# Kernel optimization log

Measured on AMD Instinct MI355X. Metric: run time of the kernel, lower is better.

The kernel has to match this reference:

```python
import jax, jax.numpy as jnp
import numpy as np

NEG_INF = -1e9

def _build_tables():
    # LC0-style 73-plane encoding per from-square: planes 0..55 queen moves
    # (8 directions x 7 distances), 56..63 knight moves. to_sq[from, plane]
    # is the to-square index; valid marks on-board targets.
    to_sq = np.zeros((64, 64), np.int32)
    valid = np.zeros((64, 64), bool)
    dirs = [(1, 0), (1, 1), (0, 1), (-1, 1), (-1, 0), (-1, -1), (0, -1), (1, -1)]
    knights = [(2, 1), (1, 2), (-1, 2), (-2, 1), (-2, -1), (-1, -2), (1, -2), (2, -1)]
    for sq in range(64):
        r, c = divmod(sq, 8)
        for d, (dr, dc) in enumerate(dirs):
            for dist in range(1, 8):
                p = d * 7 + (dist - 1)
                nr, nc = r + dr * dist, c + dc * dist
                if 0 <= nr < 8 and 0 <= nc < 8:
                    to_sq[sq, p] = nr * 8 + nc
                    valid[sq, p] = True
        for i, (dr, dc) in enumerate(knights):
            nr, nc = r + dr, c + dc
            if 0 <= nr < 8 and 0 <= nc < 8:
                to_sq[sq, 56 + i] = nr * 8 + nc
                valid[sq, 56 + i] = True
    promo_from = (np.arange(64) // 8) == 6  # rank 7 pawns (0-indexed rank 6)
    return to_sq, valid, promo_from

TO_SQ_NP, VALID_NP, PROMO_FROM_NP = _build_tables()
TO_SQ = jnp.asarray(TO_SQ_NP)            # (64, 64) int32
TO_VALID = jnp.asarray(VALID_NP)         # (64, 64) bool
PROMO_FROM = jnp.asarray(PROMO_FROM_NP)  # (64,) bool

EMBED_DIM = 1024
POLICY_DIM = 128
SCALE = POLICY_DIM ** (-0.5)


def setup_inputs() -> dict:
    key = jax.random.key(0)
    ks = jax.random.split(key, 4)
    B = 1024
    std = 1.0 / np.sqrt(EMBED_DIM)
    x = jax.random.normal(ks[0], (B, 64, EMBED_DIM), dtype=jnp.float32)
    Wq = jax.random.normal(ks[1], (EMBED_DIM, POLICY_DIM), dtype=jnp.float32) * std
    Wk = jax.random.normal(ks[2], (EMBED_DIM, POLICY_DIM), dtype=jnp.float32) * std
    Wu = jax.random.normal(ks[3], (EMBED_DIM, 9), dtype=jnp.float32) * std
    bq = jnp.zeros((POLICY_DIM,), jnp.float32)
    bk = jnp.zeros((POLICY_DIM,), jnp.float32)
    bu = jnp.zeros((9,), jnp.float32)
    return {"x": x, "Wq": Wq, "bq": bq, "Wk": Wk, "bk": bk, "Wu": Wu, "bu": bu}


def reference(x, Wq, bq, Wk, bk, Wu, bu):
    b = x.shape[0]
    q = jnp.einsum('bsd,dp->bsp', x, Wq) + bq            # (B, 64, P)
    k = jnp.einsum('bsd,dp->bsp', x, Wk) + bk            # (B, 64, P)
    logits_ft = jnp.einsum('bfp,btp->bft', q, k) * SCALE  # (B, 64, 64)
    # gather to-square logits into plane order per from-square
    idx = jnp.broadcast_to(TO_SQ[None].astype(jnp.int32), (b, 64, 64))
    logits_64 = jnp.take_along_axis(logits_ft, idx, axis=-1)  # (B, 64, 64)
    logits_64 = jnp.where(TO_VALID[None], logits_64, jnp.float32(NEG_INF))
    up = jnp.einsum('bsd,dn->bsn', x, Wu) + bu            # (B, 64, 9)
    up = jnp.where(PROMO_FROM[None, :, None], up, jnp.float32(NEG_INF))
    logits = jnp.concatenate([logits_64, up], axis=-1)    # (B, 64, 73)
    return logits.reshape(b, 64 * 73)
```

## Files before the change

### kernel.cpp

```cpp
#include <hip/hip_runtime.h>

#define NEG_INF (-1e9f)
#define SCALE_F 0.08838834764831845f

typedef __attribute__((ext_vector_type(8))) short short8;
typedef __attribute__((ext_vector_type(4))) float float4v;

__device__ __constant__ int cDR[8] = {1,1,0,-1,-1,-1,0,1};
__device__ __constant__ int cDC[8] = {0,1,1,1,0,-1,-1,-1};
__device__ __constant__ int cKR[8] = {2,1,-1,-2,-2,-1,1,2};
__device__ __constant__ int cKC[8] = {1,2,2,1,-1,-2,-2,-1};

__device__ __forceinline__ ushort f2bf(float f) {
  union { float f; unsigned u; } a; a.f = f;
  unsigned u = a.u;
  return (ushort)((u + 0x7FFFu + ((u >> 16) & 1u)) >> 16);
}

__device__ __forceinline__ short8 pack8(float4 a, float4 b) {
  union { short8 v; unsigned u[4]; } o;
  unsigned a0 = __float_as_uint(a.x), a1 = __float_as_uint(a.y);
  unsigned a2 = __float_as_uint(a.z), a3 = __float_as_uint(a.w);
  unsigned b0 = __float_as_uint(b.x), b1 = __float_as_uint(b.y);
  unsigned b2 = __float_as_uint(b.z), b3 = __float_as_uint(b.w);
  o.u[0] = (a1 & 0xFFFF0000u) | (a0 >> 16);
  o.u[1] = (a3 & 0xFFFF0000u) | (a2 >> 16);
  o.u[2] = (b1 & 0xFFFF0000u) | (b0 >> 16);
  o.u[3] = (b3 & 0xFFFF0000u) | (b2 >> 16);
  return o.v;
}

__global__ void wconv_kernel(const float* __restrict__ Wq,
                             const float* __restrict__ Wk,
                             const float* __restrict__ Wu,
                             ushort* __restrict__ Wsw) {
  int row = blockIdx.x;
  for (int k = threadIdx.x; k < 1024; k += 256) {
    float v;
    if (row < 128)      v = Wq[k * 128 + row];
    else if (row < 256) v = Wk[k * 128 + (row - 128)];
    else if (row < 265) v = Wu[k * 9 + (row - 256)];
    else                v = 0.f;
    int kc = k >> 6, kin = k & 63;
    Wsw[(size_t)kc * 18432 + row * 64 + kin] = f2bf(v);
  }
}

__global__ __launch_bounds__(256, 2)
void apol_main(const float* __restrict__ x,
               const float* __restrict__ bq,
               const float* __restrict__ bk,
               const float* __restrict__ bu,
               const ushort* __restrict__ Wsw,
               float* __restrict__ out) {
  __shared__ __align__(16) char smem[65536];
  char*   xs  = smem;
  ushort* qs  = (ushort*)smem;
  ushort* ks  = (ushort*)(smem + 16896);
  float*  Sl  = (float*)smem;

  const int tid = threadIdx.x;
  const int w = tid >> 6, lane = tid & 63;
  const int l15 = lane & 15, qd = lane >> 4;
  const char* xb = (const char*)(x + (size_t)blockIdx.x * 65536);
  const char* WsB = (const char*)Wsw;

  const int arow = l15 * 1024;
  const int axor = l15 & 7;

  const int wvo = (w * 64 + l15) * 128 + qd * 16;
  const int uvo = (256 + l15) * 128 + qd * 16;

  float4v acc[4][4];
  #pragma unroll
  for (int i = 0; i < 4; ++i)
    #pragma unroll
    for (int j = 0; j < 4; ++j)
      acc[i][j] = (float4v){0.f, 0.f, 0.f, 0.f};
  float4v aup = (float4v){0.f, 0.f, 0.f, 0.f};

  for (int h = 0; h < 2; ++h) {
    if (h) __syncthreads();
    #pragma unroll 8
    for (int j = 0; j < 16; ++j) {
      int row = j * 4 + w;
      const char* s = xb + row * 4096 + h * 2048 + lane * 32;
      float4 g0 = *(const float4*)(s);
      float4 g1 = *(const float4*)(s + 16);
      *(short8*)(xs + row * 1024 + ((lane ^ (row & 7)) * 16)) = pack8(g0, g1);
    }
    __syncthreads();

    const char* wh = WsB + (size_t)h * 8 * 36864;
    #pragma unroll 2
    for (int kc8 = 0; kc8 < 8; ++kc8) {
      const char* wp = wh + kc8 * 36864;
      #pragma unroll
      for (int kk = 0; kk < 2; ++kk) {
        short8 bf[4];
        #pragma unroll
        for (int nt = 0; nt < 4; ++nt)
          bf[nt] = *(const short8*)(wp + wvo + nt * 2048 + kk * 64);
        short8 ub;
        if (w == 3) ub = *(const short8*)(wp + uvo + kk * 64);
        #pragma unroll
        for (int mt = 0; mt < 4; ++mt) {
          short8 af = *(const short8*)(
              xs + mt * 16384 + arow + (((kc8 * 8 + kk * 4 + qd) ^ axor) * 16));
          #pragma unroll
          for (int nt = 0; nt < 4; ++nt)
            acc[mt][nt] = __builtin_amdgcn_mfma_f32_16x16x32_bf16(
                af, bf[nt], acc[mt][nt], 0, 0, 0);
          if (w == 3 && mt == 3)
            aup = __builtin_amdgcn_mfma_f32_16x16x32_bf16(af, ub, aup, 0, 0, 0);
        }
      }
    }
  }
  __syncthreads();

  float* outb = out + (size_t)blockIdx.x * 4672;

  if (w == 3 && qd < 2 && l15 < 9) {
    float bias = bu[l15];
    #pragma unroll
    for (int r = 0; r < 4; ++r) {
      int f = 48 + qd * 4 + r;
      outb[f * 73 + 64 + l15] = aup[r] + bias;
    }
  }

  #pragma unroll
  for (int nt = 0; nt < 4; ++nt) {
    int C = w * 64 + nt * 16 + l15;
    bool isq = (C < 128);
    int p = isq ? C : (C - 128);
    float bias = isq ? bq[p] : bk[p];
    ushort* dstb = isq ? qs : ks;
    #pragma unroll
    for (int mt = 0; mt < 4; ++mt)
      #pragma unroll
      for (int r = 0; r < 4; ++r) {
        int row = mt * 16 + qd * 4 + r;
        float v = acc[mt][nt][r] + bias;
        if (isq) v *= SCALE_F;
        dstb[row * 132 + p] = f2bf(v);
      }
  }
  __syncthreads();

  float4v acc2[4];
  #pragma unroll
  for (int nt = 0; nt < 4; ++nt) acc2[nt] = (float4v){0.f, 0.f, 0.f, 0.f};
  #pragma unroll
  for (int kp = 0; kp < 4; ++kp) {
    int kb = kp * 32 + qd * 8;
    short8 a2 = *(const short8*)((const char*)&qs[(w * 16 + l15) * 132 + kb]);
    #pragma unroll
    for (int nt = 0; nt < 4; ++nt) {
      short8 b2 = *(const short8*)((const char*)&ks[(nt * 16 + l15) * 132 + kb]);
      acc2[nt] = __builtin_amdgcn_mfma_f32_16x16x32_bf16(a2, b2, acc2[nt], 0, 0, 0);
    }
  }
  __syncthreads();
  #pragma unroll
  for (int nt = 0; nt < 4; ++nt)
    #pragma unroll
    for (int r = 0; r < 4; ++r)
      Sl[(w * 16 + qd * 4 + r) * 65 + nt * 16 + l15] = acc2[nt][r];
  __syncthreads();

  for (int idx = tid; idx < 4672; idx += 256) {
    int f = idx / 73;
    int j = idx - f * 73;
    float val;
    if (j < 64) {
      int rr = f >> 3, cc = f & 7;
      int nr, nc;
      if (j < 56) {
        int d = j / 7;
        int dist = j - d * 7 + 1;
        nr = rr + cDR[d] * dist;
        nc = cc + cDC[d] * dist;
      } else {
        nr = rr + cKR[j - 56];
        nc = cc + cKC[j - 56];
      }
      val = (nr >= 0 && nr < 8 && nc >= 0 && nc < 8) ? Sl[f * 65 + nr * 8 + nc]
                                                     : NEG_INF;
    } else {
      if (f >= 48 && f < 56) continue;
      val = NEG_INF;
    }
    outb[idx] = val;
  }
}

extern "C" void kernel_launch(void* const* d_in, const int* in_sizes, int n_in,
                              void* d_out, int out_size, void* d_ws, size_t ws_size,
                              hipStream_t stream) {
  const float* x  = (const float*)d_in[0];
  const float* Wq = (const float*)d_in[1];
  const float* bq = (const float*)d_in[2];
  const float* Wk = (const float*)d_in[3];
  const float* bk = (const float*)d_in[4];
  const float* Wu = (const float*)d_in[5];
  const float* bu = (const float*)d_in[6];
  float* out = (float*)d_out;
  ushort* Wsw = (ushort*)d_ws;

  const int B = in_sizes[0] / 65536;

  wconv_kernel<<<288, 256, 0, stream>>>(Wq, Wk, Wu, Wsw);
  apol_main<<<B, 256, 0, stream>>>(x, bq, bk, bu, Wsw, out);
}
```

Baseline: 447.8 us.

## Double-buffer x and weight chunks in LDS via async global_load_lds

Replaces the two-phase synchronous x staging and direct global weight loads with a 16-step K loop. Each step copies fp32 x chunks and pre-swizzled bf16 weight chunks into double-buffered LDS using global_load_lds, so the next chunk loads while the current one computes. The block grows to 512 threads, laid out as 8 waves in a 2x4 grid, at one block per CU, and x is converted to bf16 in registers at MFMA time. The aim is to hide global latency and cut register-staging overhead. In exchange it uses more LDS (104 KB), lowers occupancy, and still synchronizes once per step.

```diff
diff --git a/kernel.cpp b/kernel.cpp
--- a/kernel.cpp
+++ b/kernel.cpp
@@ -15,6 +15,12 @@
   union { float f; unsigned u; } a; a.f = f;
   unsigned u = a.u;
   return (ushort)((u + 0x7FFFu + ((u >> 16) & 1u)) >> 16);
+}
+
+__device__ __forceinline__ void glds16(const void* g, void* l) {
+  __builtin_amdgcn_global_load_lds(
+      (const __attribute__((address_space(1))) unsigned int*)g,
+      (__attribute__((address_space(3))) unsigned int*)l, 16, 0, 0);
 }
 
 __device__ __forceinline__ short8 pack8(float4 a, float4 b) {
@@ -41,87 +47,123 @@
     else if (row < 256) v = Wk[k * 128 + (row - 128)];
     else if (row < 265) v = Wu[k * 9 + (row - 256)];
     else                v = 0.f;
-    int kc = k >> 6, kin = k & 63;
-    Wsw[(size_t)kc * 18432 + row * 64 + kin] = f2bf(v);
-  }
-}
-
-__global__ __launch_bounds__(256, 2)
+    int kc = k >> 6, kin = k & 63, seg = kin >> 3, j = kin & 7;
+    int sseg = seg ^ (row & 7);
+    Wsw[(size_t)kc * 18432 + row * 64 + sseg * 8 + j] = f2bf(v);
+  }
+}
+
+__global__ __launch_bounds__(512, 1)
 void apol_main(const float* __restrict__ x,
                const float* __restrict__ bq,
                const float* __restrict__ bk,
                const float* __restrict__ bu,
                const ushort* __restrict__ Wsw,
                float* __restrict__ out) {
-  __shared__ __align__(16) char smem[65536];
-  char*   xs  = smem;
+  __shared__ __align__(16) char smem[106496];
+  char*   xs0 = smem;
+  char*   xs1 = smem + 16384;
+  char*   wt0 = smem + 32768;
+  char*   wt1 = smem + 69632;
   ushort* qs  = (ushort*)smem;
   ushort* ks  = (ushort*)(smem + 16896);
   float*  Sl  = (float*)smem;
 
   const int tid = threadIdx.x;
-  const int w = tid >> 6, lane = tid & 63;
+  const int wv = tid >> 6, lane = tid & 63;
   const int l15 = lane & 15, qd = lane >> 4;
+  const int wr = wv >> 2, wc = wv & 3;
   const char* xb = (const char*)(x + (size_t)blockIdx.x * 65536);
   const char* WsB = (const char*)Wsw;
 
-  const int arow = l15 * 1024;
-  const int axor = l15 & 7;
-
-  const int wvo = (w * 64 + l15) * 128 + qd * 16;
-  const int uvo = (256 + l15) * 128 + qd * 16;
-
-  float4v acc[4][4];
-  #pragma unroll
-  for (int i = 0; i < 4; ++i)
+  const int xsrow = lane >> 4;
+  const int xgran = lane & 15;
+
+  int arowb[2];
+  #pragma unroll
+  for (int mt = 0; mt < 2; ++mt) arowb[mt] = (wr * 32 + mt * 16 + l15) * 256;
+  int agr[2][2];
+  #pragma unroll
+  for (int kk = 0; kk < 2; ++kk)
+    #pragma unroll
+    for (int h = 0; h < 2; ++h)
+      agr[kk][h] = (((kk * 8 + qd * 2 + h) ^ (l15 & 7)) * 16);
+
+  int brow[4];
+  #pragma unroll
+  for (int nt = 0; nt < 4; ++nt) brow[nt] = (wc * 64 + nt * 16 + l15) * 128;
+  const int urow = (256 + l15) * 128;
+  int bgr[2];
+  #pragma unroll
+  for (int kk = 0; kk < 2; ++kk)
+    bgr[kk] = (((kk * 4 + qd) ^ (l15 & 7)) * 16);
+
+  float4v acc[2][4];
+  #pragma unroll
+  for (int i = 0; i < 2; ++i)
     #pragma unroll
     for (int j = 0; j < 4; ++j)
       acc[i][j] = (float4v){0.f, 0.f, 0.f, 0.f};
   float4v aup = (float4v){0.f, 0.f, 0.f, 0.f};
 
-  for (int h = 0; h < 2; ++h) {
-    if (h) __syncthreads();
-    #pragma unroll 8
-    for (int j = 0; j < 16; ++j) {
-      int row = j * 4 + w;
-      const char* s = xb + row * 4096 + h * 2048 + lane * 32;
-      float4 g0 = *(const float4*)(s);
-      float4 g1 = *(const float4*)(s + 16);
-      *(short8*)(xs + row * 1024 + ((lane ^ (row & 7)) * 16)) = pack8(g0, g1);
-    }
+#define STAGE(KC, XD, WD)                                                      \
+  {                                                                            \
+    _Pragma("unroll")                                                          \
+    for (int c = 0; c < 7; ++c) {                                              \
+      int slot = c * 8 + wv;                                                   \
+      if (slot < 16) {                                                         \
+        int r = slot * 4 + xsrow;                                              \
+        glds16(xb + r * 4096 + (KC) * 256 + ((xgran ^ (r & 7)) * 16),          \
+               (XD) + slot * 1024);                                            \
+      } else if (slot < 52) {                                                  \
+        glds16(WsB + (size_t)(KC) * 36864 + (slot - 16) * 1024 + lane * 16,    \
+               (WD) + (slot - 16) * 1024);                                     \
+      }                                                                        \
+    }                                                                          \
+  }
+
+#define COMPUTE(XC, WC)                                                        \
+  {                                                                            \
+    _Pragma("unroll")                                                          \
+    for (int kk = 0; kk < 2; ++kk) {                                           \
+      short8 bf[4];                                                            \
+      _Pragma("unroll")                                                        \
+      for (int nt = 0; nt < 4; ++nt)                                           \
+        bf[nt] = *(const short8*)((WC) + brow[nt] + bgr[kk]);                  \
+      short8 ub;                                                               \
+      if (wv == 7) ub = *(const short8*)((WC) + urow + bgr[kk]);               \
+      _Pragma("unroll")                                                        \
+      for (int mt = 0; mt < 2; ++mt) {                                         \
+        float4 g0 = *(const float4*)((XC) + arowb[mt] + agr[kk][0]);           \
+        float4 g1 = *(const float4*)((XC) + arowb[mt] + agr[kk][1]);           \
+        short8 af = pack8(g0, g1);                                             \
+        _Pragma("unroll")                                                      \
+        for (int nt = 0; nt < 4; ++nt)                                         \
+          acc[mt][nt] = __builtin_amdgcn_mfma_f32_16x16x32_bf16(               \
+              af, bf[nt], acc[mt][nt], 0, 0, 0);                               \
+        if (wv == 7 && mt == 1)                                                \
+          aup = __builtin_amdgcn_mfma_f32_16x16x32_bf16(af, ub, aup, 0, 0, 0); \
+      }                                                                        \
+    }                                                                          \
+  }
+
+  STAGE(0, xs0, wt0);
+  __syncthreads();
+  #pragma unroll 1
+  for (int kc = 0; kc < 16; kc += 2) {
+    STAGE(kc + 1, xs1, wt1);
+    COMPUTE(xs0, wt0);
     __syncthreads();
-
-    const char* wh = WsB + (size_t)h * 8 * 36864;
-    #pragma unroll 2
-    for (int kc8 = 0; kc8 < 8; ++kc8) {
-      const char* wp = wh + kc8 * 36864;
-      #pragma unroll
-      for (int kk = 0; kk < 2; ++kk) {
-        short8 bf[4];
-        #pragma unroll
-        for (int nt = 0; nt < 4; ++nt)
-          bf[nt] = *(const short8*)(wp + wvo + nt * 2048 + kk * 64);
-        short8 ub;
-        if (w == 3) ub = *(const short8*)(wp + uvo + kk * 64);
-        #pragma unroll
-        for (int mt = 0; mt < 4; ++mt) {
-          short8 af = *(const short8*)(
-              xs + mt * 16384 + arow + (((kc8 * 8 + kk * 4 + qd) ^ axor) * 16));
-          #pragma unroll
-          for (int nt = 0; nt < 4; ++nt)
-            acc[mt][nt] = __builtin_amdgcn_mfma_f32_16x16x32_bf16(
-                af, bf[nt], acc[mt][nt], 0, 0, 0);
-          if (w == 3 && mt == 3)
-            aup = __builtin_amdgcn_mfma_f32_16x16x32_bf16(af, ub, aup, 0, 0, 0);
-        }
-      }
-    }
-  }
-  __syncthreads();
+    if (kc < 14) STAGE(kc + 2, xs0, wt0);
+    COMPUTE(xs1, wt1);
+    __syncthreads();
+  }
+#undef STAGE
+#undef COMPUTE
 
   float* outb = out + (size_t)blockIdx.x * 4672;
 
-  if (w == 3 && qd < 2 && l15 < 9) {
+  if (wv == 7 && qd < 2 && l15 < 9) {
     float bias = bu[l15];
     #pragma unroll
     for (int r = 0; r < 4; ++r) {
@@ -132,16 +174,16 @@
 
   #pragma unroll
   for (int nt = 0; nt < 4; ++nt) {
-    int C = w * 64 + nt * 16 + l15;
+    int C = wc * 64 + nt * 16 + l15;
     bool isq = (C < 128);
     int p = isq ? C : (C - 128);
     float bias = isq ? bq[p] : bk[p];
     ushort* dstb = isq ? qs : ks;
     #pragma unroll
-    for (int mt = 0; mt < 4; ++mt)
+    for (int mt = 0; mt < 2; ++mt)
       #pragma unroll
       for (int r = 0; r < 4; ++r) {
-        int row = mt * 16 + qd * 4 + r;
+        int row = wr * 32 + mt * 16 + qd * 4 + r;
         float v = acc[mt][nt][r] + bias;
         if (isq) v *= SCALE_F;
         dstb[row * 132 + p] = f2bf(v);
@@ -149,28 +191,30 @@
   }
   __syncthreads();
 
-  float4v acc2[4];
-  #pragma unroll
-  for (int nt = 0; nt < 4; ++nt) acc2[nt] = (float4v){0.f, 0.f, 0.f, 0.f};
+  const int r16 = wv >> 1, c32 = wv & 1;
+  float4v acc2[2];
+  acc2[0] = (float4v){0.f, 0.f, 0.f, 0.f};
+  acc2[1] = (float4v){0.f, 0.f, 0.f, 0.f};
   #pragma unroll
   for (int kp = 0; kp < 4; ++kp) {
     int kb = kp * 32 + qd * 8;
-    short8 a2 = *(const short8*)((const char*)&qs[(w * 16 + l15) * 132 + kb]);
-    #pragma unroll
-    for (int nt = 0; nt < 4; ++nt) {
-      short8 b2 = *(const short8*)((const char*)&ks[(nt * 16 + l15) * 132 + kb]);
+    short8 a2 = *(const short8*)((const char*)&qs[(r16 * 16 + l15) * 132 + kb]);
+    #pragma unroll
+    for (int nt = 0; nt < 2; ++nt) {
+      short8 b2 = *(const short8*)(
+          (const char*)&ks[((c32 * 2 + nt) * 16 + l15) * 132 + kb]);
       acc2[nt] = __builtin_amdgcn_mfma_f32_16x16x32_bf16(a2, b2, acc2[nt], 0, 0, 0);
     }
   }
   __syncthreads();
   #pragma unroll
-  for (int nt = 0; nt < 4; ++nt)
+  for (int nt = 0; nt < 2; ++nt)
     #pragma unroll
     for (int r = 0; r < 4; ++r)
-      Sl[(w * 16 + qd * 4 + r) * 65 + nt * 16 + l15] = acc2[nt][r];
-  __syncthreads();
-
-  for (int idx = tid; idx < 4672; idx += 256) {
+      Sl[(r16 * 16 + qd * 4 + r) * 65 + (c32 * 2 + nt) * 16 + l15] = acc2[nt][r];
+  __syncthreads();
+
+  for (int idx = tid; idx < 4672; idx += 512) {
     int f = idx / 73;
     int j = idx - f * 73;
     float val;
@@ -212,5 +256,5 @@
   const int B = in_sizes[0] / 65536;
 
   wconv_kernel<<<288, 256, 0, stream>>>(Wq, Wk, Wu, Wsw);
-  apol_main<<<B, 256, 0, stream>>>(x, bq, bk, bu, Wsw, out);
-}
+  apol_main<<<B, 512, 0, stream>>>(x, bq, bk, bu, Wsw, out);
+}
```

After: 441.8 us. No clear change (-1.3%).
